# Kernel optimization log

Hardware: AMD Instinct MI355X
Metric: run time of the kernel (lower is better)

## Reference

```python
import jax, jax.numpy as jnp
import numpy as np

B, S, FEAT = 4, 512, 16
D, H, L, DFF, NC, RPH = 512, 8, 6, 2048, 12, 64
DH = D // H
CLAMP = 5.0
LN_EPS = 1e-5
STD_EPS = 1e-6


def setup_inputs() -> dict:
    key = jax.random.key(0)
    ks = iter(jax.random.split(key, 32))
    sc = lambda *shape: 0.02 * jax.random.normal(next(ks), shape, dtype=jnp.float32)
    inp = {
        "x": jax.random.normal(next(ks), (B, S, FEAT), dtype=jnp.float32),
        # RelPosBias2D MLP: Linear(2,RPH) -> ReLU -> Linear(RPH,H)
        "relpos_w1": sc(RPH, 2), "relpos_b1": jnp.zeros((RPH,), jnp.float32),
        "relpos_w2": sc(H, RPH), "relpos_b2": jnp.zeros((H,), jnp.float32),
        "embed_w": sc(D, FEAT), "embed_b": jnp.zeros((D,), jnp.float32),
        # per-layer params stacked on leading L axis
        "attn_in_w": sc(L, 3 * D, D), "attn_in_b": jnp.zeros((L, 3 * D), jnp.float32),
        "attn_out_w": sc(L, D, D), "attn_out_b": jnp.zeros((L, D), jnp.float32),
        "ff_w1": sc(L, DFF, D), "ff_b1": jnp.zeros((L, DFF), jnp.float32),
        "ff_w2": sc(L, D, DFF), "ff_b2": jnp.zeros((L, D), jnp.float32),
        "ln1_s": jnp.ones((L, D), jnp.float32), "ln1_b": jnp.zeros((L, D), jnp.float32),
        "ln2_s": jnp.ones((L, D), jnp.float32), "ln2_b": jnp.zeros((L, D), jnp.float32),
        "fc_w": sc(NC, D), "fc_b": jnp.zeros((NC,), jnp.float32),
    }
    return inp


def _standardize(v):  # (B,S), unmasked path of _masked_standardize
    mean = v.mean(axis=1, keepdims=True)
    var = ((v - mean) ** 2).mean(axis=1, keepdims=True)
    return (v - mean) / jnp.sqrt(var + STD_EPS)


def _layernorm(v, s, b):
    mean = v.mean(axis=-1, keepdims=True)
    var = ((v - mean) ** 2).mean(axis=-1, keepdims=True)
    return (v - mean) * jax.lax.rsqrt(var + LN_EPS) * s + b


def reference(x, relpos_w1, relpos_b1, relpos_w2, relpos_b2, embed_w, embed_b,
              attn_in_w, attn_in_b, attn_out_w, attn_out_b,
              ff_w1, ff_b1, ff_w2, ff_b2, ln1_s, ln1_b, ln2_s, ln2_b, fc_w, fc_b):
    # --- 2D relative position bias ---
    t = _standardize(x[..., 0])
    f = _standardize(x[..., 1])
    dt = t[:, :, None] - t[:, None, :]          # (B,S,S)
    df = f[:, :, None] - f[:, None, :]
    rel = jnp.stack([dt, df], axis=-1)           # (B,S,S,2)
    hid = jax.nn.relu(rel @ relpos_w1.T + relpos_b1)
    bias = hid @ relpos_w2.T + relpos_b2         # (B,S,S,H)
    bias = jnp.clip(bias, -CLAMP, CLAMP)
    bias = jnp.transpose(bias, (0, 3, 1, 2))     # (B,H,S,S)

    h = x @ embed_w.T + embed_b                  # (B,S,D)
    scale = 1.0 / jnp.sqrt(jnp.float32(DH))
    for l in range(L):
        qkv = h @ attn_in_w[l].T + attn_in_b[l]  # (B,S,3D)
        q, k, v = jnp.split(qkv, 3, axis=-1)
        q = q.reshape(B, S, H, DH)
        k = k.reshape(B, S, H, DH)
        v = v.reshape(B, S, H, DH)
        scores = jnp.einsum('bihd,bjhd->bhij', q, k) * scale + bias
        attn = jax.nn.softmax(scores, axis=-1)
        o = jnp.einsum('bhij,bjhd->bihd', attn, v).reshape(B, S, D)
        o = o @ attn_out_w[l].T + attn_out_b[l]
        h = _layernorm(h + o, ln1_s[l], ln1_b[l])
        ff = jax.nn.relu(h @ ff_w1[l].T + ff_b1[l]) @ ff_w2[l].T + ff_b2[l]
        h = _layernorm(h + ff, ln2_s[l], ln2_b[l])

    rep = h.mean(axis=1)                         # mean pooling, no mask
    return rep @ fc_w.T + fc_b                   # (B,NC)
```

## Files before the change

### kernel.cpp

```cpp
#include <hip/hip_runtime.h>
#include <hip/hip_bf16.h>
#include <stdint.h>

using short8 = __attribute__((ext_vector_type(8))) short;
using us4    = __attribute__((ext_vector_type(4))) unsigned short;
using f32x4  = __attribute__((ext_vector_type(4))) float;
using bf16   = __hip_bfloat16;

constexpr int CB=4, CS=512, CF=16, CD=512, CH=8, CL=6, CDFF=2048, CNC=12, CRPH=64, CDH=64;

__device__ inline void gload_lds16(const void* g, void* l) {
    __builtin_amdgcn_global_load_lds((const __attribute__((address_space(1))) void*)g,
                                     (__attribute__((address_space(3))) void*)l, 16, 0, 0);
}
__device__ inline float bfbits2f(unsigned short u) {
    return __uint_as_float(((uint32_t)u) << 16);
}
__device__ inline unsigned short f2bfbits(float f) {
    return __builtin_bit_cast(unsigned short, __float2bfloat16(f));
}

template<int BM, int BN, int TPB>
struct MMGeom {
    static constexpr int WC  = (TPB == 512) ? 4 : 2;
    static constexpr int WR  = (TPB/64)/WC;
    static constexpr int RS  = BM/WR;
    static constexpr int CSP = BN/WC;
    static constexpr int MR  = RS/16;
    static constexpr int NR  = CSP/16;
    static constexpr int NLD = (BM+BN)*128/(TPB*16);
};

template<int BM, int BN, int TPB>
__device__ inline void stage_tile(const bf16* A, int lda, const bf16* W, int ldw, int k0,
                                  char* As, char* Bs) {
    constexpr int AC = (BM*128)/(TPB*16);
    constexpr int BC = (BN*128)/(TPB*16);
    const int tid = threadIdx.x;
#pragma unroll
    for (int i = 0; i < AC; i++) {
        int s = i*TPB + tid;
        int r = s >> 3, u = s & 7;
        const char* gp = (const char*)(A + (size_t)r*lda + k0) + ((u ^ (r&7))*16);
        gload_lds16(gp, As + (size_t)(s & ~63)*16);
    }
#pragma unroll
    for (int i = 0; i < BC; i++) {
        int s = i*TPB + tid;
        int r = s >> 3, u = s & 7;
        const char* gp = (const char*)(W + (size_t)r*ldw + k0) + ((u ^ (r&7))*16);
        gload_lds16(gp, Bs + (size_t)(s & ~63)*16);
    }
}

template<int BM, int BN, int TPB>
__device__ inline void compute_tile64(const char* As, const char* Bs,
                                      int wr, int wc, int c, int g,
                                      f32x4 (&acc)[MMGeom<BM,BN,TPB>::MR][MMGeom<BM,BN,TPB>::NR]) {
    using G = MMGeom<BM,BN,TPB>;
#pragma unroll
    for (int kk = 0; kk < 2; kk++) {
        short8 af[G::MR], bfv[G::NR];
#pragma unroll
        for (int m = 0; m < G::MR; m++) {
            int row = wr*G::RS + m*16 + c;
            af[m] = *(const short8*)(As + row*128 + (((kk*4+g) ^ (row&7))*16));
        }
#pragma unroll
        for (int n = 0; n < G::NR; n++) {
            int row = wc*G::CSP + n*16 + c;
            bfv[n] = *(const short8*)(Bs + row*128 + (((kk*4+g) ^ (row&7))*16));
        }
#pragma unroll
        for (int m = 0; m < G::MR; m++)
#pragma unroll
            for (int n = 0; n < G::NR; n++)
                acc[m][n] = __builtin_amdgcn_mfma_f32_16x16x32_bf16(af[m], bfv[n], acc[m][n], 0, 0, 0);
    }
}

template<int BM, int BN, int TPB>
__device__ inline void mm_core_pipe(const bf16* A, int lda, const bf16* W, int ldw, int K,
                                    char* smem,
                                    f32x4 (&acc)[MMGeom<BM,BN,TPB>::MR][MMGeom<BM,BN,TPB>::NR]) {
    using G = MMGeom<BM,BN,TPB>;
    constexpr int SSZ = (BM+BN)*128;
    const int tid = threadIdx.x;
    const int lane = tid & 63, wv = tid >> 6;
    const int wr = wv / G::WC, wc = wv % G::WC;
    const int g = lane >> 4, c = lane & 15;

    const int nk = K >> 6;
    stage_tile<BM,BN,TPB>(A, lda, W, ldw, 0, smem, smem + BM*128);
    if (nk > 1) stage_tile<BM,BN,TPB>(A, lda, W, ldw, 64, smem + SSZ, smem + SSZ + BM*128);

    for (int t = 0; t < nk; t++) {
        char* bc = smem + (size_t)(t & 3)*SSZ;
        if (t + 2 < nk) {
            char* bs = smem + (size_t)((t+2) & 3)*SSZ;
            stage_tile<BM,BN,TPB>(A, lda, W, ldw, (t+2)*64, bs, bs + BM*128);
            asm volatile("s_waitcnt vmcnt(%0)" :: "n"(2*G::NLD) : "memory");
        } else if (t + 1 < nk) {
            asm volatile("s_waitcnt vmcnt(%0)" :: "n"(G::NLD) : "memory");
        } else {
            asm volatile("s_waitcnt vmcnt(0)" ::: "memory");
        }
        __builtin_amdgcn_s_barrier();
        compute_tile64<BM,BN,TPB>(bc, bc + BM*128, wr, wc, c, g, acc);
    }
}

template<int BM, int BN, int EPI, int KSPLIT, int TPB>
__global__ __launch_bounds__(TPB) void k_mm(const bf16* __restrict__ A, int lda,
                                            const bf16* __restrict__ W, int ldw,
                                            const float* __restrict__ bias,
                                            bf16* __restrict__ Cb, float* __restrict__ Cf,
                                            int ldc, int K) {
    using G = MMGeom<BM,BN,TPB>;
    __shared__ char smem[4*(BM+BN)*128];
    const int bm = blockIdx.y * BM, bn = blockIdx.x * BN;
    const int kz = (KSPLIT > 1) ? blockIdx.z : 0;
    const int Kper = K / KSPLIT;
    f32x4 acc[G::MR][G::NR] = {};
    mm_core_pipe<BM,BN,TPB>(A + (size_t)bm*lda + kz*Kper, lda,
                            W + (size_t)bn*ldw + kz*Kper, ldw, Kper, smem, acc);
    const int lane = threadIdx.x & 63, wv = threadIdx.x >> 6;
    const int wr = wv / G::WC, wc = wv % G::WC;
    const int g = lane >> 4, c = lane & 15;
    float* Cfz = Cf + (size_t)kz * 2048 * ldc;
#pragma unroll
    for (int m = 0; m < G::MR; m++)
#pragma unroll
        for (int n = 0; n < G::NR; n++)
#pragma unroll
            for (int j = 0; j < 4; j++) {
                int row = bm + wr*G::RS + m*16 + g*4 + j;
                int col = bn + wc*G::CSP + n*16 + c;
                float v = acc[m][n][j] + ((kz == 0) ? bias[col] : 0.0f);
                if (EPI == 1) v = fmaxf(v, 0.0f);
                if (EPI == 2) Cfz[(size_t)row*ldc + col] = v;
                else          Cb[(size_t)row*ldc + col] = __float2bfloat16(v);
            }
}

__global__ __launch_bounds__(512) void k_mm_qkv(const bf16* __restrict__ A,
                                                const bf16* __restrict__ W,
                                                const float* __restrict__ bias,
                                                bf16* __restrict__ qkvb,
                                                bf16* __restrict__ vtb) {
    constexpr int BM = 128, BN = 128, TPB = 512;
    using G = MMGeom<BM,BN,TPB>;
    __shared__ char smem[4*(BM+BN)*128];
    const int bm = blockIdx.y * BM, bn = blockIdx.x * BN;
    f32x4 acc[G::MR][G::NR] = {};
    mm_core_pipe<BM,BN,TPB>(A + (size_t)bm*CD, CD, W + (size_t)bn*CD, CD, CD, smem, acc);
    const int lane = threadIdx.x & 63, wv = threadIdx.x >> 6;
    const int wr = wv / G::WC, wc = wv % G::WC;
    const int g = lane >> 4, c = lane & 15;
    if (bn < 2*CD) {
#pragma unroll
        for (int m = 0; m < G::MR; m++)
#pragma unroll
            for (int n = 0; n < G::NR; n++)
#pragma unroll
                for (int j = 0; j < 4; j++) {
                    int row = bm + wr*G::RS + m*16 + g*4 + j;
                    int col = bn + wc*G::CSP + n*16 + c;
                    qkvb[(size_t)row*(3*CD) + col] = __float2bfloat16(acc[m][n][j] + bias[col]);
                }
    } else {
#pragma unroll
        for (int m = 0; m < G::MR; m++)
#pragma unroll
            for (int n = 0; n < G::NR; n++) {
                int row0 = bm + wr*G::RS + m*16 + g*4;
                int col  = bn + wc*G::CSP + n*16 + c;
                int z = (row0 >> 9)*8 + ((col - 2*CD) >> 6);
                int d = (col - 2*CD) & 63;
                int s0 = row0 & 511;
                float bcol = bias[col];
                us4 o;
#pragma unroll
                for (int j = 0; j < 4; j++) o[j] = f2bfbits(acc[m][n][j] + bcol);
                *(us4*)(vtb + ((size_t)z*CDH + d)*CS + s0) = o;
            }
    }
}

__global__ __launch_bounds__(256) void k_attn_fused(const bf16* __restrict__ qkv,
                                                    const bf16* __restrict__ vt,
                                                    const bf16* __restrict__ bias,
                                                    bf16* __restrict__ att) {
    __shared__ char Ksm[4][16384];
    __shared__ char Vsm[4][16384];
    __shared__ char Ps[16384];

    const int z = blockIdx.y, b = z >> 3, h = z & 7;
    const int qbase = blockIdx.x * 64;
    const int tid = threadIdx.x, l = tid & 63, w = tid >> 6;
    const int g = l >> 4, c = l & 15, swz = l & 7;
    const int q_global = qbase + w*16 + c;

    const bf16* qrow = qkv + ((size_t)(b*CS + q_global))*(3*CD) + h*CDH;
    short8 bq0 = *(const short8*)(qrow + g*8);
    short8 bq1 = *(const short8*)(qrow + 32 + g*8);
    const bf16* brow = bias + ((size_t)z*CS + q_global)*CS;

    float mrun = -1e30f, lsum = 0.0f;
    f32x4 accO[4] = {};
    char* Pb = Ps + w*4096;

    auto stageKV = [&](int kv0, char* Ks, char* Vs) {
#pragma unroll
        for (int i = 0; i < 4; i++) {
            int s = i*256 + tid;
            int r = s >> 3, u = s & 7;
            const bf16* gk = qkv + ((size_t)(b*CS + kv0 + r))*(3*CD) + CD + h*CDH + ((u ^ (r&7)) * 8);
            gload_lds16(gk, Ks + (size_t)(s & ~63)*16);
        }
#pragma unroll
        for (int i = 0; i < 4; i++) {
            int s = i*256 + tid;
            int d = s >> 4, u = s & 15;
            const bf16* gv = vt + ((size_t)(z*CDH + d))*CS + kv0 + ((u ^ (d&7)) * 8);
            gload_lds16(gv, Vs + (size_t)(s & ~63)*16);
        }
    };

    stageKV(0,   Ksm[0], Vsm[0]);
    stageKV(128, Ksm[1], Vsm[1]);

    for (int t = 0; t < 4; t++) {
        int kv0 = t * 128;
        if (t < 2) stageKV((t+2)*128, Ksm[t+2], Vsm[t+2]);
        if (t == 0)      asm volatile("s_waitcnt vmcnt(32)" ::: "memory");
        else if (t == 1) asm volatile("s_waitcnt vmcnt(40)" ::: "memory");
        else if (t == 2) asm volatile("s_waitcnt vmcnt(32)" ::: "memory");
        else             asm volatile("s_waitcnt vmcnt(16)" ::: "memory");
        __builtin_amdgcn_s_barrier();
        const char* Kc = Ksm[t];
        const char* Vc = Vsm[t];

        float sv[8][4];
        float tmax = -1e30f;
#pragma unroll
        for (int n = 0; n < 8; n++) {
            int row = n*16 + c;
            short8 af0 = *(const short8*)(Kc + row*128 + ((g    ^ swz) * 16));
            short8 af1 = *(const short8*)(Kc + row*128 + (((4+g) ^ swz) * 16));
            f32x4 a = {};
            a = __builtin_amdgcn_mfma_f32_16x16x32_bf16(af0, bq0, a, 0, 0, 0);
            a = __builtin_amdgcn_mfma_f32_16x16x32_bf16(af1, bq1, a, 0, 0, 0);
            us4 b4 = *(const us4*)(brow + kv0 + n*16 + g*4);
#pragma unroll
            for (int j = 0; j < 4; j++) {
                sv[n][j] = a[j] * 0.125f + bfbits2f(b4[j]);
                tmax = fmaxf(tmax, sv[n][j]);
            }
        }
        tmax = fmaxf(tmax, __shfl_xor(tmax, 16));
        tmax = fmaxf(tmax, __shfl_xor(tmax, 32));
        if (!__all(tmax - mrun <= 8.0f)) {
            float mnew = fmaxf(mrun, tmax);
            float corr = __expf(mrun - mnew);
            lsum *= corr;
#pragma unroll
            for (int n2 = 0; n2 < 4; n2++)
#pragma unroll
                for (int j = 0; j < 4; j++) accO[n2][j] *= corr;
            mrun = mnew;
        }
        float tsum = 0.0f;
#pragma unroll
        for (int n = 0; n < 8; n++)
#pragma unroll
            for (int j = 0; j < 4; j++) {
                float e = __expf(sv[n][j] - mrun);
                sv[n][j] = e;
                tsum += e;
            }
        tsum += __shfl_xor(tsum, 16);
        tsum += __shfl_xor(tsum, 32);
        lsum += tsum;

#pragma unroll
        for (int n = 0; n < 8; n++) {
            us4 pk;
#pragma unroll
            for (int j = 0; j < 4; j++) pk[j] = f2bfbits(sv[n][j]);
            *(us4*)(Pb + c*256 + ((n*32 + g*8) ^ (swz << 4))) = pk;
        }

#pragma unroll
        for (int n2 = 0; n2 < 4; n2++) {
            int d = n2*16 + c;
#pragma unroll
            for (int kk = 0; kk < 4; kk++) {
                short8 av = *(const short8*)(Vc + d*256 + (((kk*4 + g) ^ swz) * 16));
                short8 bp = *(const short8*)(Pb + c*256 + (((kk*64 + g*16) ^ (swz << 4))));
                accO[n2] = __builtin_amdgcn_mfma_f32_16x16x32_bf16(av, bp, accO[n2], 0, 0, 0);
            }
        }
    }

    float inv = 1.0f / lsum;
    bf16* orow = att + ((size_t)(b*CS + q_global))*CD + h*CDH;
#pragma unroll
    for (int n2 = 0; n2 < 4; n2++) {
        us4 o;
#pragma unroll
        for (int j = 0; j < 4; j++) o[j] = f2bfbits(accO[n2][j] * inv);
        *(us4*)(orow + n2*16 + g*4) = o;
    }
}

__global__ void k_standardize(const float* __restrict__ x, float* __restrict__ ts,
                              float* __restrict__ fs) {
    int b = blockIdx.x, ch = blockIdx.y, tid = threadIdx.x;
    __shared__ float red[256];
    float v0 = x[(b*CS + tid)*CF + ch];
    float v1 = x[(b*CS + tid + 256)*CF + ch];
    red[tid] = v0 + v1; __syncthreads();
    for (int w = 128; w > 0; w >>= 1) { if (tid < w) red[tid] += red[tid+w]; __syncthreads(); }
    float mean = red[0] * (1.0f/CS); __syncthreads();
    float d0 = v0-mean, d1 = v1-mean;
    red[tid] = d0*d0 + d1*d1; __syncthreads();
    for (int w = 128; w > 0; w >>= 1) { if (tid < w) red[tid] += red[tid+w]; __syncthreads(); }
    float inv = rsqrtf(red[0]*(1.0f/CS) + 1e-6f);
    float* o = ch == 0 ? ts : fs;
    o[b*CS + tid] = d0*inv; o[b*CS + tid + 256] = d1*inv;
}

__global__ __launch_bounds__(256) void k_relpos(const float* __restrict__ ts, const float* __restrict__ fs,
                         const float* __restrict__ w1, const float* __restrict__ b1,
                         const float* __restrict__ w2, const float* __restrict__ b2,
                         bf16* __restrict__ bias) {
    int idx = blockIdx.x * 256 + threadIdx.x;
    int j = idx & (CS-1), i = (idx >> 9) & (CS-1), b = idx >> 18;
    float dt = ts[b*CS + i] - ts[b*CS + j];
    float df = fs[b*CS + i] - fs[b*CS + j];
    float acc[CH];
#pragma unroll
    for (int h = 0; h < CH; h++) acc[h] = b2[h];
    for (int r = 0; r < CRPH; r++) {
        float hd = fmaxf(w1[r*2]*dt + w1[r*2+1]*df + b1[r], 0.0f);
#pragma unroll
        for (int h = 0; h < CH; h++) acc[h] += w2[h*CRPH + r] * hd;
    }
#pragma unroll
    for (int h = 0; h < CH; h++) {
        float v = fminf(fmaxf(acc[h], -5.0f), 5.0f);
        bias[((size_t)(b*CH + h)*CS + i)*CS + j] = __float2bfloat16(v);
    }
}

__global__ __launch_bounds__(256) void k_embed(const float* __restrict__ x, const float* __restrict__ w,
                        const float* __restrict__ bv, float* __restrict__ h, bf16* __restrict__ hb) {
    int idx = blockIdx.x * 256 + threadIdx.x;
    int d = idx & (CD-1), m = idx >> 9;
    const float* xr = x + m*CF;
    const float* wr = w + d*CF;
    float acc = bv[d];
#pragma unroll
    for (int f = 0; f < CF; f++) acc += xr[f]*wr[f];
    h[idx] = acc; hb[idx] = __float2bfloat16(acc);
}

template<int NADD>
__global__ __launch_bounds__(256) void k_ln(float* __restrict__ h, const float* __restrict__ a0,
                     const float* __restrict__ a1,
                     const float* __restrict__ s, const float* __restrict__ bv, bf16* __restrict__ hb) {
    const int w = threadIdx.x >> 6, l = threadIdx.x & 63;
    const int row = blockIdx.x*4 + w;
    float* hr = h + (size_t)row*CD;
    const float* ar = a0 + (size_t)row*CD;
    const float* a1r = (NADD == 2) ? (a1 + (size_t)row*CD) : nullptr;

    float v[8];
    {
        float4 h0 = ((const float4*)hr)[l*2],  h1 = ((const float4*)hr)[l*2+1];
        float4 b0 = ((const float4*)ar)[l*2],  b1 = ((const float4*)ar)[l*2+1];
        v[0]=h0.x+b0.x; v[1]=h0.y+b0.y; v[2]=h0.z+b0.z; v[3]=h0.w+b0.w;
        v[4]=h1.x+b1.x; v[5]=h1.y+b1.y; v[6]=h1.z+b1.z; v[7]=h1.w+b1.w;
        if (NADD == 2) {
            float4 c0 = ((const float4*)a1r)[l*2], c1 = ((const float4*)a1r)[l*2+1];
            v[0]+=c0.x; v[1]+=c0.y; v[2]+=c0.z; v[3]+=c0.w;
            v[4]+=c1.x; v[5]+=c1.y; v[6]+=c1.z; v[7]+=c1.w;
        }
    }
    float sum = 0.f, sq = 0.f;
#pragma unroll
    for (int i = 0; i < 8; i++) { sum += v[i]; sq += v[i]*v[i]; }
#pragma unroll
    for (int off = 1; off < 64; off <<= 1) {
        sum += __shfl_xor(sum, off);
        sq  += __shfl_xor(sq, off);
    }
    float mean = sum * (1.0f/CD);
    float var  = sq * (1.0f/CD) - mean*mean;
    float rstd = rsqrtf(var + 1e-5f);

    float4 s0 = ((const float4*)s)[l*2],  s1 = ((const float4*)s)[l*2+1];
    float4 g0 = ((const float4*)bv)[l*2], g1 = ((const float4*)bv)[l*2+1];
    float o[8];
    o[0]=(v[0]-mean)*rstd*s0.x+g0.x; o[1]=(v[1]-mean)*rstd*s0.y+g0.y;
    o[2]=(v[2]-mean)*rstd*s0.z+g0.z; o[3]=(v[3]-mean)*rstd*s0.w+g0.w;
    o[4]=(v[4]-mean)*rstd*s1.x+g1.x; o[5]=(v[5]-mean)*rstd*s1.y+g1.y;
    o[6]=(v[6]-mean)*rstd*s1.z+g1.z; o[7]=(v[7]-mean)*rstd*s1.w+g1.w;

    ((float4*)hr)[l*2]   = make_float4(o[0],o[1],o[2],o[3]);
    ((float4*)hr)[l*2+1] = make_float4(o[4],o[5],o[6],o[7]);
    short8 ob;
#pragma unroll
    for (int i = 0; i < 8; i++) ob[i] = (short)f2bfbits(o[i]);
    *(short8*)(hb + (size_t)row*CD + l*8) = ob;
}

__global__ __launch_bounds__(256) void k_wconv(const float* __restrict__ a0, const float* __restrict__ a1,
                        const float* __restrict__ a2, const float* __restrict__ a3,
                        bf16* __restrict__ dst) {
    size_t i = ((size_t)blockIdx.x * 256 + threadIdx.x) * 8;
    const float* src; size_t off;
    if (i < 786432)       { src = a0; off = i; }
    else if (i < 1048576) { src = a1; off = i - 786432; }
    else if (i < 2097152) { src = a2; off = i - 1048576; }
    else                  { src = a3; off = i - 2097152; }
    short8 o;
#pragma unroll
    for (int j = 0; j < 8; j++) o[j] = __builtin_bit_cast(short, __float2bfloat16(src[off + j]));
    *(short8*)(void*)(dst + i) = o;
}

__global__ __launch_bounds__(256) void k_wconv_all(const float* __restrict__ aiw, const float* __restrict__ aow,
                        const float* __restrict__ f1w, const float* __restrict__ f2w,
                        bf16* __restrict__ dst) {
    int lyr = blockIdx.y;
    size_t i = ((size_t)blockIdx.x * 256 + threadIdx.x) * 8;
    const float* src; size_t off;
    if (i < 786432)       { src = aiw + (size_t)lyr* 786432; off = i; }
    else if (i < 1048576) { src = aow + (size_t)lyr* 262144; off = i - 786432; }
    else if (i < 2097152) { src = f1w + (size_t)lyr*1048576; off = i - 1048576; }
    else                  { src = f2w + (size_t)lyr*1048576; off = i - 2097152; }
    short8 o;
#pragma unroll
    for (int j = 0; j < 8; j++) o[j] = __builtin_bit_cast(short, __float2bfloat16(src[off + j]));
    *(short8*)(void*)(dst + (size_t)lyr*3145728 + i) = o;
}

__global__ __launch_bounds__(256) void k_pool(const float* __restrict__ h, float* __restrict__ rep) {
    int b = blockIdx.x, d0 = blockIdx.y * 64;
    int t = threadIdx.x, dl = t & 63, sg = t >> 6;
    float acc = 0.0f;
    for (int s = sg*128; s < sg*128 + 128; s++)
        acc += h[((size_t)(b*CS + s))*CD + d0 + dl];
    __shared__ float red[256];
    red[t] = acc; __syncthreads();
    if (t < 64)
        rep[b*CD + d0 + dl] = (red[t] + red[t+64] + red[t+128] + red[t+192]) * (1.0f/CS);
}

__global__ void k_fc(const float* __restrict__ rep, const float* __restrict__ fcw,
                     const float* __restrict__ fcb, float* __restrict__ out) {
    int b = blockIdx.x, cc = blockIdx.y, l = threadIdx.x;
    float acc = 0.0f;
    for (int d = l; d < CD; d += 64) acc += rep[b*CD + d] * fcw[cc*CD + d];
    for (int o = 32; o > 0; o >>= 1) acc += __shfl_xor(acc, o);
    if (l == 0) out[b*CNC + cc] = acc + fcb[cc];
}

extern "C" void kernel_launch(void* const* d_in, const int* in_sizes, int n_in,
                              void* d_out, int out_size, void* d_ws, size_t ws_size,
                              hipStream_t stream) {
    const float* x   = (const float*)d_in[0];
    const float* rw1 = (const float*)d_in[1];
    const float* rb1 = (const float*)d_in[2];
    const float* rw2 = (const float*)d_in[3];
    const float* rb2 = (const float*)d_in[4];
    const float* emw = (const float*)d_in[5];
    const float* emb = (const float*)d_in[6];
    const float* aiw = (const float*)d_in[7];
    const float* aib = (const float*)d_in[8];
    const float* aow = (const float*)d_in[9];
    const float* aob = (const float*)d_in[10];
    const float* f1w = (const float*)d_in[11];
    const float* f1b = (const float*)d_in[12];
    const float* f2w = (const float*)d_in[13];
    const float* f2b = (const float*)d_in[14];
    const float* l1s = (const float*)d_in[15];
    const float* l1b = (const float*)d_in[16];
    const float* l2s = (const float*)d_in[17];
    const float* l2b = (const float*)d_in[18];
    const float* fcw = (const float*)d_in[19];
    const float* fcb = (const float*)d_in[20];
    float* out = (float*)d_out;

    char* p = (char*)d_ws;
    auto alloc = [&](size_t bytes) { char* r = p; p += (bytes + 255) & ~(size_t)255; return r; };
    bf16*  biasb = (bf16*)alloc((size_t)CB*CH*CS*CS*2);
    float* h     = (float*)alloc((size_t)CB*CS*CD*4);
    bf16*  hb    = (bf16*)alloc((size_t)CB*CS*CD*2);
    bf16*  qkvb  = (bf16*)alloc((size_t)CB*CS*3*CD*2);
    bf16*  vtb   = (bf16*)alloc((size_t)CB*CH*CDH*CS*2);
    bf16*  attb  = (bf16*)alloc((size_t)CB*CS*CD*2);
    float* tmp   = (float*)alloc((size_t)2*CB*CS*CD*4);
    bf16*  ffb   = (bf16*)alloc((size_t)CB*CS*CDFF*2);
    bf16*  wl    = (bf16*)alloc((size_t)3145728*2);
    float* rep   = (float*)alloc((size_t)CB*CD*4);
    float* ts    = (float*)alloc(CB*CS*4);
    float* fs    = (float*)alloc(CB*CS*4);

    size_t used = (size_t)(p - (char*)d_ws);
    const size_t WLE = 3145728;
    bool oneshot = (ws_size > used) && ((ws_size - used) >= (size_t)CL*WLE*2 + 256);
    bf16* wlall = (bf16*)alloc(oneshot ? (size_t)CL*WLE*2 : 0);

    const int M = CB*CS;
    float* tmp2 = tmp + (size_t)M*CD;

    k_standardize<<<dim3(CB,2), 256, 0, stream>>>(x, ts, fs);
    k_relpos<<<(CB*CS*CS)/256, 256, 0, stream>>>(ts, fs, rw1, rb1, rw2, rb2, biasb);
    k_embed<<<(M*CD)/256, 256, 0, stream>>>(x, emw, emb, h, hb);
    if (oneshot)
        k_wconv_all<<<dim3(1536, CL), 256, 0, stream>>>(aiw, aow, f1w, f2w, wlall);

    for (int l = 0; l < CL; l++) {
        const bf16* wbase = oneshot ? (wlall + (size_t)l*WLE) : wl;
        if (!oneshot)
            k_wconv<<<1536, 256, 0, stream>>>(aiw + (size_t)l*786432, aow + (size_t)l*262144,
                                              f1w + (size_t)l*1048576, f2w + (size_t)l*1048576, wl);
        const bf16* wl_aiw = wbase;
        const bf16* wl_aow = wbase + 786432;
        const bf16* wl_f1w = wbase + 1048576;
        const bf16* wl_f2w = wbase + 2097152;
        k_mm_qkv<<<dim3(12,16), 512, 0, stream>>>(hb, wl_aiw, aib + (size_t)l*3*CD, qkvb, vtb);
        k_attn_fused<<<dim3(CS/64, CB*CH), 256, 0, stream>>>(qkvb, vtb, biasb, attb);
        k_mm<64,64,2,1,512><<<dim3(8,32), 512, 0, stream>>>(attb, CD, wl_aow, CD,
                                                            aob + (size_t)l*CD, nullptr, tmp, CD, CD);
        k_ln<1><<<M/4, 256, 0, stream>>>(h, tmp, nullptr, l1s + (size_t)l*CD, l1b + (size_t)l*CD, hb);
        k_mm<128,128,1,1,512><<<dim3(16,16), 512, 0, stream>>>(hb, CD, wl_f1w, CD,
                                                               f1b + (size_t)l*CDFF, ffb, nullptr, CDFF, CD);
        k_mm<64,64,2,2,512><<<dim3(8,32,2), 512, 0, stream>>>(ffb, CDFF, wl_f2w, CDFF,
                                                              f2b + (size_t)l*CD, nullptr, tmp, CD, CDFF);
        k_ln<2><<<M/4, 256, 0, stream>>>(h, tmp, tmp2, l2s + (size_t)l*CD, l2b + (size_t)l*CD, hb);
    }

    k_pool<<<dim3(CB, CD/64), 256, 0, stream>>>(h, rep);
    k_fc<<<dim3(CB, CNC), 64, 0, stream>>>(rep, fcw, fcb, out);
}
```

Before: 457.8 us.

## Fuse residual add and LayerNorm into projection GEMMs via last-block row reduction

Removes the separate LayerNorm kernels by fusing the residual add, bias and row statistics into the attention-out and FF2 GEMM epilogues. Each block writes its pre-norm tile to a temp buffer and atomically adds per-row sum and sum of squares into global buffers. A per-row-block counter lets the last block to finish normalise the full rows and write h and hb. The FF2 split-K across two slices is dropped, so that GEMM now runs over the full K=2048 with half the blocks, and the attention kernel's final wait becomes vmcnt(0). This adds global atomics, fences and one extra memset, and the last block does serialized normalisation work.

New measurement: 833.1 us. 1.82x slower.

```diff
diff --git a/kernel.cpp b/kernel.cpp
--- a/kernel.cpp
+++ b/kernel.cpp
@@ -110,24 +110,19 @@
     }
 }
 
-template<int BM, int BN, int EPI, int KSPLIT, int TPB>
+template<int BM, int BN, int EPI, int TPB>
 __global__ __launch_bounds__(TPB) void k_mm(const bf16* __restrict__ A, int lda,
                                             const bf16* __restrict__ W, int ldw,
                                             const float* __restrict__ bias,
-                                            bf16* __restrict__ Cb, float* __restrict__ Cf,
-                                            int ldc, int K) {
+                                            bf16* __restrict__ Cb, int ldc, int K) {
     using G = MMGeom<BM,BN,TPB>;
     __shared__ char smem[4*(BM+BN)*128];
     const int bm = blockIdx.y * BM, bn = blockIdx.x * BN;
-    const int kz = (KSPLIT > 1) ? blockIdx.z : 0;
-    const int Kper = K / KSPLIT;
     f32x4 acc[G::MR][G::NR] = {};
-    mm_core_pipe<BM,BN,TPB>(A + (size_t)bm*lda + kz*Kper, lda,
-                            W + (size_t)bn*ldw + kz*Kper, ldw, Kper, smem, acc);
+    mm_core_pipe<BM,BN,TPB>(A + (size_t)bm*lda, lda, W + (size_t)bn*ldw, ldw, K, smem, acc);
     const int lane = threadIdx.x & 63, wv = threadIdx.x >> 6;
     const int wr = wv / G::WC, wc = wv % G::WC;
     const int g = lane >> 4, c = lane & 15;
-    float* Cfz = Cf + (size_t)kz * 2048 * ldc;
 #pragma unroll
     for (int m = 0; m < G::MR; m++)
 #pragma unroll
@@ -136,11 +131,110 @@
             for (int j = 0; j < 4; j++) {
                 int row = bm + wr*G::RS + m*16 + g*4 + j;
                 int col = bn + wc*G::CSP + n*16 + c;
-                float v = acc[m][n][j] + ((kz == 0) ? bias[col] : 0.0f);
+                float v = acc[m][n][j] + bias[col];
                 if (EPI == 1) v = fmaxf(v, 0.0f);
-                if (EPI == 2) Cfz[(size_t)row*ldc + col] = v;
-                else          Cb[(size_t)row*ldc + col] = __float2bfloat16(v);
+                Cb[(size_t)row*ldc + col] = __float2bfloat16(v);
             }
+}
+
+__global__ __launch_bounds__(512) void k_mm_lnfix(const bf16* __restrict__ A, int lda,
+                                                  const bf16* __restrict__ W, int ldw, int K,
+                                                  const float* __restrict__ bias,
+                                                  float* __restrict__ h, bf16* __restrict__ hb,
+                                                  float* __restrict__ tmp,
+                                                  const float* __restrict__ lns,
+                                                  const float* __restrict__ lnb,
+                                                  float* __restrict__ Ssum,
+                                                  float* __restrict__ Qsum,
+                                                  unsigned int* __restrict__ cnt) {
+    constexpr int BM = 64, BN = 64, TPB = 512;
+    using G = MMGeom<BM,BN,TPB>;
+    __shared__ char smem[4*(BM+BN)*128];
+    __shared__ float lsS[BM], lsQ[BM];
+    __shared__ unsigned int s_old;
+
+    const int bm = blockIdx.y * BM, bn = blockIdx.x * BN;
+    const int tid = threadIdx.x;
+    const int lane = tid & 63, wv = tid >> 6;
+    const int wr = wv / G::WC, wc = wv % G::WC;
+    const int g = lane >> 4, c = lane & 15;
+
+    f32x4 acc[G::MR][G::NR] = {};
+    mm_core_pipe<BM,BN,TPB>(A + (size_t)bm*lda, lda, W + (size_t)bn*ldw, ldw, K, smem, acc);
+
+    if (tid < BM) { lsS[tid] = 0.0f; lsQ[tid] = 0.0f; }
+    __syncthreads();
+
+    float s_[2][4], q_[2][4];
+#pragma unroll
+    for (int m = 0; m < 2; m++)
+#pragma unroll
+        for (int j = 0; j < 4; j++) {
+            int rl = wr*32 + m*16 + g*4 + j;
+            int col = bn + wc*16 + c;
+            float x = acc[m][0][j] + bias[col] + h[(size_t)(bm+rl)*CD + col];
+            tmp[(size_t)(bm+rl)*CD + col] = x;
+            s_[m][j] = x; q_[m][j] = x*x;
+        }
+#pragma unroll
+    for (int m = 0; m < 2; m++)
+#pragma unroll
+        for (int j = 0; j < 4; j++)
+#pragma unroll
+            for (int off = 1; off < 16; off <<= 1) {
+                s_[m][j] += __shfl_xor(s_[m][j], off);
+                q_[m][j] += __shfl_xor(q_[m][j], off);
+            }
+    if (c == 0) {
+#pragma unroll
+        for (int m = 0; m < 2; m++)
+#pragma unroll
+            for (int j = 0; j < 4; j++) {
+                int rl = wr*32 + m*16 + g*4 + j;
+                atomicAdd(&lsS[rl], s_[m][j]);
+                atomicAdd(&lsQ[rl], q_[m][j]);
+            }
+    }
+    __syncthreads();
+    if (tid < BM) {
+        atomicAdd(&Ssum[bm + tid], lsS[tid]);
+        atomicAdd(&Qsum[bm + tid], lsQ[tid]);
+    }
+    __syncthreads();
+    if (tid == 0) {
+        __builtin_amdgcn_fence(__ATOMIC_RELEASE, "agent");
+        s_old = __hip_atomic_fetch_add(&cnt[blockIdx.y], 1u, __ATOMIC_ACQ_REL,
+                                       __HIP_MEMORY_SCOPE_AGENT);
+    }
+    __syncthreads();
+    if (s_old == 7) {
+        __builtin_amdgcn_fence(__ATOMIC_ACQUIRE, "agent");
+        int r = tid >> 3, cc0 = (tid & 7) * 64;
+        int row = bm + r;
+        float S = Ssum[row], Q = Qsum[row];
+        float mean = S * (1.0f/CD);
+        float var  = Q * (1.0f/CD) - mean*mean;
+        float rstd = rsqrtf(var + 1e-5f);
+        for (int c4 = 0; c4 < 64; c4 += 4) {
+            int col = cc0 + c4;
+            float4 x = *(const float4*)&tmp[(size_t)row*CD + col];
+            float4 sc = *(const float4*)&lns[col];
+            float4 bc = *(const float4*)&lnb[col];
+            float4 y;
+            y.x = (x.x-mean)*rstd*sc.x + bc.x;
+            y.y = (x.y-mean)*rstd*sc.y + bc.y;
+            y.z = (x.z-mean)*rstd*sc.z + bc.z;
+            y.w = (x.w-mean)*rstd*sc.w + bc.w;
+            *(float4*)&h[(size_t)row*CD + col] = y;
+            us4 ob;
+            ob[0] = f2bfbits(y.x); ob[1] = f2bfbits(y.y);
+            ob[2] = f2bfbits(y.z); ob[3] = f2bfbits(y.w);
+            *(us4*)(hb + (size_t)row*CD + col) = ob;
+        }
+        if ((tid & 7) == 0) { Ssum[row] = 0.0f; Qsum[row] = 0.0f; }
+        if (tid == 0)
+            __hip_atomic_store(&cnt[blockIdx.y], 0u, __ATOMIC_RELAXED, __HIP_MEMORY_SCOPE_AGENT);
+    }
 }
 
 __global__ __launch_bounds__(512) void k_mm_qkv(const bf16* __restrict__ A,
@@ -236,7 +330,7 @@
         if (t == 0)      asm volatile("s_waitcnt vmcnt(32)" ::: "memory");
         else if (t == 1) asm volatile("s_waitcnt vmcnt(40)" ::: "memory");
         else if (t == 2) asm volatile("s_waitcnt vmcnt(32)" ::: "memory");
-        else             asm volatile("s_waitcnt vmcnt(16)" ::: "memory");
+        else             asm volatile("s_waitcnt vmcnt(0)" ::: "memory");
         __builtin_amdgcn_s_barrier();
         const char* Kc = Ksm[t];
         const char* Vc = Vsm[t];
@@ -366,71 +460,6 @@
     h[idx] = acc; hb[idx] = __float2bfloat16(acc);
 }
 
-template<int NADD>
-__global__ __launch_bounds__(256) void k_ln(float* __restrict__ h, const float* __restrict__ a0,
-                     const float* __restrict__ a1,
-                     const float* __restrict__ s, const float* __restrict__ bv, bf16* __restrict__ hb) {
-    const int w = threadIdx.x >> 6, l = threadIdx.x & 63;
-    const int row = blockIdx.x*4 + w;
-    float* hr = h + (size_t)row*CD;
-    const float* ar = a0 + (size_t)row*CD;
-    const float* a1r = (NADD == 2) ? (a1 + (size_t)row*CD) : nullptr;
-
-    float v[8];
-    {
-        float4 h0 = ((const float4*)hr)[l*2],  h1 = ((const float4*)hr)[l*2+1];
-        float4 b0 = ((const float4*)ar)[l*2],  b1 = ((const float4*)ar)[l*2+1];
-        v[0]=h0.x+b0.x; v[1]=h0.y+b0.y; v[2]=h0.z+b0.z; v[3]=h0.w+b0.w;
-        v[4]=h1.x+b1.x; v[5]=h1.y+b1.y; v[6]=h1.z+b1.z; v[7]=h1.w+b1.w;
-        if (NADD == 2) {
-            float4 c0 = ((const float4*)a1r)[l*2], c1 = ((const float4*)a1r)[l*2+1];
-            v[0]+=c0.x; v[1]+=c0.y; v[2]+=c0.z; v[3]+=c0.w;
-            v[4]+=c1.x; v[5]+=c1.y; v[6]+=c1.z; v[7]+=c1.w;
-        }
-    }
-    float sum = 0.f, sq = 0.f;
-#pragma unroll
-    for (int i = 0; i < 8; i++) { sum += v[i]; sq += v[i]*v[i]; }
-#pragma unroll
-    for (int off = 1; off < 64; off <<= 1) {
-        sum += __shfl_xor(sum, off);
-        sq  += __shfl_xor(sq, off);
-    }
-    float mean = sum * (1.0f/CD);
-    float var  = sq * (1.0f/CD) - mean*mean;
-    float rstd = rsqrtf(var + 1e-5f);
-
-    float4 s0 = ((const float4*)s)[l*2],  s1 = ((const float4*)s)[l*2+1];
-    float4 g0 = ((const float4*)bv)[l*2], g1 = ((const float4*)bv)[l*2+1];
-    float o[8];
-    o[0]=(v[0]-mean)*rstd*s0.x+g0.x; o[1]=(v[1]-mean)*rstd*s0.y+g0.y;
-    o[2]=(v[2]-mean)*rstd*s0.z+g0.z; o[3]=(v[3]-mean)*rstd*s0.w+g0.w;
-    o[4]=(v[4]-mean)*rstd*s1.x+g1.x; o[5]=(v[5]-mean)*rstd*s1.y+g1.y;
-    o[6]=(v[6]-mean)*rstd*s1.z+g1.z; o[7]=(v[7]-mean)*rstd*s1.w+g1.w;
-
-    ((float4*)hr)[l*2]   = make_float4(o[0],o[1],o[2],o[3]);
-    ((float4*)hr)[l*2+1] = make_float4(o[4],o[5],o[6],o[7]);
-    short8 ob;
-#pragma unroll
-    for (int i = 0; i < 8; i++) ob[i] = (short)f2bfbits(o[i]);
-    *(short8*)(hb + (size_t)row*CD + l*8) = ob;
-}
-
-__global__ __launch_bounds__(256) void k_wconv(const float* __restrict__ a0, const float* __restrict__ a1,
-                        const float* __restrict__ a2, const float* __restrict__ a3,
-                        bf16* __restrict__ dst) {
-    size_t i = ((size_t)blockIdx.x * 256 + threadIdx.x) * 8;
-    const float* src; size_t off;
-    if (i < 786432)       { src = a0; off = i; }
-    else if (i < 1048576) { src = a1; off = i - 786432; }
-    else if (i < 2097152) { src = a2; off = i - 1048576; }
-    else                  { src = a3; off = i - 2097152; }
-    short8 o;
-#pragma unroll
-    for (int j = 0; j < 8; j++) o[j] = __builtin_bit_cast(short, __float2bfloat16(src[off + j]));
-    *(short8*)(void*)(dst + i) = o;
-}
-
 __global__ __launch_bounds__(256) void k_wconv_all(const float* __restrict__ aiw, const float* __restrict__ aow,
                         const float* __restrict__ f1w, const float* __restrict__ f2w,
                         bf16* __restrict__ dst) {
@@ -445,6 +474,21 @@
 #pragma unroll
     for (int j = 0; j < 8; j++) o[j] = __builtin_bit_cast(short, __float2bfloat16(src[off + j]));
     *(short8*)(void*)(dst + (size_t)lyr*3145728 + i) = o;
+}
+
+__global__ __launch_bounds__(256) void k_wconv(const float* __restrict__ a0, const float* __restrict__ a1,
+                        const float* __restrict__ a2, const float* __restrict__ a3,
+                        bf16* __restrict__ dst) {
+    size_t i = ((size_t)blockIdx.x * 256 + threadIdx.x) * 8;
+    const float* src; size_t off;
+    if (i < 786432)       { src = a0; off = i; }
+    else if (i < 1048576) { src = a1; off = i - 786432; }
+    else if (i < 2097152) { src = a2; off = i - 1048576; }
+    else                  { src = a3; off = i - 2097152; }
+    short8 o;
+#pragma unroll
+    for (int j = 0; j < 8; j++) o[j] = __builtin_bit_cast(short, __float2bfloat16(src[off + j]));
+    *(short8*)(void*)(dst + i) = o;
 }
 
 __global__ __launch_bounds__(256) void k_pool(const float* __restrict__ h, float* __restrict__ rep) {
@@ -502,12 +546,17 @@
     bf16*  qkvb  = (bf16*)alloc((size_t)CB*CS*3*CD*2);
     bf16*  vtb   = (bf16*)alloc((size_t)CB*CH*CDH*CS*2);
     bf16*  attb  = (bf16*)alloc((size_t)CB*CS*CD*2);
-    float* tmp   = (float*)alloc((size_t)2*CB*CS*CD*4);
+    float* tmp   = (float*)alloc((size_t)CB*CS*CD*4);
     bf16*  ffb   = (bf16*)alloc((size_t)CB*CS*CDFF*2);
     bf16*  wl    = (bf16*)alloc((size_t)3145728*2);
     float* rep   = (float*)alloc((size_t)CB*CD*4);
     float* ts    = (float*)alloc(CB*CS*4);
     float* fs    = (float*)alloc(CB*CS*4);
+    float* Ssum  = (float*)alloc((size_t)CB*CS*4);
+    float* Qsum  = (float*)alloc((size_t)CB*CS*4);
+    unsigned int* cnt = (unsigned int*)alloc(32*4);
+    char* syncbase = (char*)Ssum;
+    size_t syncbytes = (size_t)((char*)p - syncbase);
 
     size_t used = (size_t)(p - (char*)d_ws);
     const size_t WLE = 3145728;
@@ -515,8 +564,8 @@
     bf16* wlall = (bf16*)alloc(oneshot ? (size_t)CL*WLE*2 : 0);
 
     const int M = CB*CS;
-    float* tmp2 = tmp + (size_t)M*CD;
-
+
+    hipMemsetAsync(syncbase, 0, syncbytes, stream);
     k_standardize<<<dim3(CB,2), 256, 0, stream>>>(x, ts, fs);
     k_relpos<<<(CB*CS*CS)/256, 256, 0, stream>>>(ts, fs, rw1, rb1, rw2, rb2, biasb);
     k_embed<<<(M*CD)/256, 256, 0, stream>>>(x, emw, emb, h, hb);
@@ -534,14 +583,16 @@
         const bf16* wl_f2w = wbase + 2097152;
         k_mm_qkv<<<dim3(12,16), 512, 0, stream>>>(hb, wl_aiw, aib + (size_t)l*3*CD, qkvb, vtb);
         k_attn_fused<<<dim3(CS/64, CB*CH), 256, 0, stream>>>(qkvb, vtb, biasb, attb);
-        k_mm<64,64,2,1,512><<<dim3(8,32), 512, 0, stream>>>(attb, CD, wl_aow, CD,
-                                                            aob + (size_t)l*CD, nullptr, tmp, CD, CD);
-        k_ln<1><<<M/4, 256, 0, stream>>>(h, tmp, nullptr, l1s + (size_t)l*CD, l1b + (size_t)l*CD, hb);
-        k_mm<128,128,1,1,512><<<dim3(16,16), 512, 0, stream>>>(hb, CD, wl_f1w, CD,
-                                                               f1b + (size_t)l*CDFF, ffb, nullptr, CDFF, CD);
-        k_mm<64,64,2,2,512><<<dim3(8,32,2), 512, 0, stream>>>(ffb, CDFF, wl_f2w, CDFF,
-                                                              f2b + (size_t)l*CD, nullptr, tmp, CD, CDFF);
-        k_ln<2><<<M/4, 256, 0, stream>>>(h, tmp, tmp2, l2s + (size_t)l*CD, l2b + (size_t)l*CD, hb);
+        k_mm_lnfix<<<dim3(8,32), 512, 0, stream>>>(attb, CD, wl_aow, CD, CD,
+                                                   aob + (size_t)l*CD, h, hb, tmp,
+                                                   l1s + (size_t)l*CD, l1b + (size_t)l*CD,
+                                                   Ssum, Qsum, cnt);
+        k_mm<128,128,1,512><<<dim3(16,16), 512, 0, stream>>>(hb, CD, wl_f1w, CD,
+                                                             f1b + (size_t)l*CDFF, ffb, CDFF, CD);
+        k_mm_lnfix<<<dim3(8,32), 512, 0, stream>>>(ffb, CDFF, wl_f2w, CDFF, CDFF,
+                                                   f2b + (size_t)l*CD, h, hb, tmp,
+                                                   l2s + (size_t)l*CD, l2b + (size_t)l*CD,
+                                                   Ssum, Qsum, cnt);
     }
 
     k_pool<<<dim3(CB, CD/64), 256, 0, stream>>>(h, rep);
```
